# Optimization experiments

Measured on AMD Instinct MI355X. Metric: run time of the kernel, lower is better.

Reference implementation:

```python
import jax, jax.numpy as jnp
import numpy as np

THRESH = 0.5
MARGIN = 0.1
SCALE_POS = 2.0
SCALE_NEG = 40.0
EPS = 1e-5


def setup_inputs() -> dict:
    key = jax.random.key(0)
    k1, k2 = jax.random.split(key)
    B, D, NUM_CLASSES = 4096, 512, 512
    feats = jax.random.normal(k1, (B, D), dtype=jnp.float32)
    feats = feats / jnp.linalg.norm(feats, axis=1, keepdims=True)  # unit-norm embeddings
    labels = jax.random.randint(k2, (B,), 0, NUM_CLASSES, dtype=jnp.int64)
    return {"feats": feats, "labels": labels, "label_num": 26}


def reference(feats, labels, label_num):
    B = feats.shape[0]
    sim = feats @ feats.T  # [B, B]
    same = labels[:, None] == labels[None, :]
    pos_m = same & (sim < 1.0 - EPS)      # pos_pair_ mask per row
    neg_m = ~same                         # neg_pair_ mask per row
    has_pos = pos_m.any(axis=1)
    has_neg = neg_m.any(axis=1)
    min_pos = jnp.min(jnp.where(pos_m, sim, jnp.inf), axis=1)
    max_neg = jnp.max(jnp.where(neg_m, sim, -jnp.inf), axis=1)
    pos_thr = jnp.where(has_pos, min_pos, jnp.float32(0.2))  # fallback when no pos pairs
    neg_thr = jnp.where(has_neg, max_neg, jnp.float32(0.8))  # fallback when no neg pairs
    # mined pairs (same semantics as the per-row boolean filtering)
    neg_pair = neg_m & (sim + MARGIN > pos_thr[:, None])
    pos_pair = pos_m & (sim - MARGIN < neg_thr[:, None])
    valid = pos_pair.any(axis=1) & neg_pair.any(axis=1) & (jnp.arange(B) < B - label_num)
    # masked log-sum-exp style reductions (exp of -inf on masked entries -> 0)
    pos_sum = jnp.sum(jnp.exp(jnp.where(pos_pair, -SCALE_POS * (sim - THRESH), -jnp.inf)), axis=1)
    neg_sum = jnp.sum(jnp.exp(jnp.where(neg_pair, SCALE_NEG * (sim - THRESH), -jnp.inf)), axis=1)
    per_row = (1.0 / SCALE_POS) * jnp.log1p(pos_sum) + (1.0 / SCALE_NEG) * jnp.log1p(neg_sum)
    return jnp.sum(jnp.where(valid, per_row, 0.0)) / B
```

## Files before the change

### kernel.cpp

```cpp
#include <hip/hip_runtime.h>
#include <stdint.h>

#define BN 4096
#define DK 512
#define THRESH 0.5f
#define MARGIN 0.1f

typedef __attribute__((ext_vector_type(8))) __bf16 bf16x8;
typedef __attribute__((ext_vector_type(4))) float f32x4;
typedef __attribute__((ext_vector_type(8))) unsigned short ushort8;

__device__ __forceinline__ unsigned short f2bf(float f) {
    unsigned u = __float_as_uint(f);
    u += 0x7FFFu + ((u >> 16) & 1u);
    return (unsigned short)(u >> 16);
}
__device__ __forceinline__ float bf2f(unsigned short b) {
    return __uint_as_float((unsigned)b << 16);
}

__device__ __forceinline__ void async_cp16(void* lds, const void* g) {
    __builtin_amdgcn_global_load_lds(
        (const __attribute__((address_space(1))) void*)g,
        (__attribute__((address_space(3))) void*)lds,
        16, 0, 0);
}

__global__ void cvt_kernel(const float4* __restrict__ in, ushort4* __restrict__ out,
                           float* __restrict__ loss_out) {
    int i = blockIdx.x * blockDim.x + threadIdx.x;
    float4 v = in[i];
    ushort4 o;
    o.x = f2bf(v.x); o.y = f2bf(v.y); o.z = f2bf(v.z); o.w = f2bf(v.w);
    out[i] = o;
    if (blockIdx.x == 0 && threadIdx.x == 0) loss_out[0] = 0.f;
}

__global__ __launch_bounds__(256, 4) void ms_gemm(
    const unsigned short* __restrict__ Fb,
    unsigned short* __restrict__ simb)
{
    __shared__ __align__(16) unsigned short SMEM[2 * 128 * 64];
    unsigned short* As = SMEM;
    unsigned short* Bs = SMEM + 128 * 64;

    const int t    = threadIdx.x;
    const int lane = t & 63;
    const int w    = t >> 6;
    const int wr   = w >> 1, wc = w & 1;
    const int quad = lane >> 4;
    const int cIdx = lane & 15;

    int l = blockIdx.x, by = 0;
    while (l >= 32 - by) { l -= (32 - by); ++by; }
    const int bx = by + l;
    const int rowBase = by * 128;
    const int colBase = bx * 128;

    f32x4 acc[4][4];
#pragma unroll
    for (int i = 0; i < 4; ++i)
#pragma unroll
        for (int j = 0; j < 4; ++j) acc[i][j] = (f32x4){0.f, 0.f, 0.f, 0.f};

    const int lrow   = t >> 3;
    const int swz    = (t & 7) ^ (lrow & 7);
    const int ldsOff = t * 8;

    for (int k0 = 0; k0 < DK; k0 += 64) {
#pragma unroll
        for (int it = 0; it < 4; ++it) {
            const unsigned short* gA =
                Fb + (size_t)(rowBase + it * 32 + lrow) * DK + k0 + swz * 8;
            async_cp16(&As[it * 2048 + ldsOff], gA);
        }
#pragma unroll
        for (int it = 0; it < 4; ++it) {
            const unsigned short* gB =
                Fb + (size_t)(colBase + it * 32 + lrow) * DK + k0 + swz * 8;
            async_cp16(&Bs[it * 2048 + ldsOff], gB);
        }
        __syncthreads();

#pragma unroll
        for (int kk = 0; kk < 2; ++kk) {
            bf16x8 af[4], bg[4];
#pragma unroll
            for (int im = 0; im < 4; ++im) {
                int r = wr * 64 + im * 16 + cIdx;
                int p = (kk * 4 + quad) ^ (r & 7);
                af[im] = *reinterpret_cast<const bf16x8*>(&As[r * 64 + p * 8]);
            }
#pragma unroll
            for (int jn = 0; jn < 4; ++jn) {
                int c = wc * 64 + jn * 16 + cIdx;
                int p = (kk * 4 + quad) ^ (c & 7);
                bg[jn] = *reinterpret_cast<const bf16x8*>(&Bs[c * 64 + p * 8]);
            }
#pragma unroll
            for (int im = 0; im < 4; ++im)
#pragma unroll
                for (int jn = 0; jn < 4; ++jn)
                    acc[im][jn] = __builtin_amdgcn_mfma_f32_16x16x32_bf16(
                        af[im], bg[jn], acc[im][jn], 0, 0, 0);
        }
        __syncthreads();
    }

#pragma unroll
    for (int im = 0; im < 4; ++im)
#pragma unroll
        for (int rg = 0; rg < 4; ++rg) {
            const int grow = rowBase + wr * 64 + im * 16 + quad * 4 + rg;
            unsigned short* dst = simb + (size_t)grow * BN + colBase + wc * 64 + cIdx;
#pragma unroll
            for (int jn = 0; jn < 4; ++jn)
                dst[jn * 16] = f2bf(acc[im][jn][rg]);
        }

    if (by == bx) return;

#pragma unroll
    for (int im = 0; im < 4; ++im)
#pragma unroll
        for (int jn = 0; jn < 4; ++jn) {
            ushort4 v;
            v.x = f2bf(acc[im][jn][0]);
            v.y = f2bf(acc[im][jn][1]);
            v.z = f2bf(acc[im][jn][2]);
            v.w = f2bf(acc[im][jn][3]);
            const int c  = wc * 64 + jn * 16 + cIdx;
            const int r  = wr * 64 + im * 16 + quad * 4;
            const int r8 = r >> 3;
            const int ri = r & 7;
            *reinterpret_cast<ushort4*>(
                &SMEM[c * 128 + ((r8 ^ (c & 15)) << 3) + ri]) = v;
        }
    __syncthreads();

    const int lch = t & 7;
    const int trw = t >> 3;
#pragma unroll
    for (int it = 0; it < 4; ++it) {
        const int tr = it * 32 + trw;
        const int q1 = lch ^ (tr & 15);
        const int q2 = (lch + 8) ^ (tr & 15);
        ushort8 a = *reinterpret_cast<const ushort8*>(&SMEM[tr * 128 + q1 * 8]);
        ushort8 b = *reinterpret_cast<const ushort8*>(&SMEM[tr * 128 + q2 * 8]);
        unsigned short* dst = simb + (size_t)(colBase + tr) * BN + rowBase;
        *reinterpret_cast<ushort8*>(&dst[lch * 8])       = a;
        *reinterpret_cast<ushort8*>(&dst[(lch + 8) * 8]) = b;
    }
}

__global__ __launch_bounds__(256) void ms_rows(
    const unsigned short* __restrict__ simb,
    const int* __restrict__ labels,
    const int* __restrict__ label_num,
    float* __restrict__ out)
{
    __shared__ int   labS[BN];
    __shared__ float bsum[4];

    const int t    = threadIdx.x;
    const int lane = t & 63;
    const int w    = t >> 6;

    for (int i = t; i < BN; i += 256) labS[i] = labels[i];
    __syncthreads();

    const int lim = BN - label_num[0];
    const int row = blockIdx.x * 4 + w;
    const int lr  = labS[row];
    const ushort8* rp = (const ushort8*)(simb + (size_t)row * BN);

    ushort8 d[8];
    uint64_t mpos = 0, msame = 0;
    float mn = INFINITY, mx = -INFINITY;
#pragma unroll
    for (int j = 0; j < 8; ++j) {
        d[j] = rp[j * 64 + lane];
#pragma unroll
        for (int e = 0; e < 8; ++e) {
            const int col = (j * 64 + lane) * 8 + e;
            const float s = bf2f(d[j][e]);
            const bool same = (labS[col] == lr);
            const bool pos  = same && (col != row);
            if (pos)   mn = fminf(mn, s);
            if (!same) mx = fmaxf(mx, s);
            msame |= (uint64_t)same << (j * 8 + e);
            mpos  |= (uint64_t)pos  << (j * 8 + e);
        }
    }
#pragma unroll
    for (int off = 1; off < 64; off <<= 1) {
        mn = fminf(mn, __shfl_xor(mn, off, 64));
        mx = fmaxf(mx, __shfl_xor(mx, off, 64));
    }
    const float tP = (mn < 1e30f)  ? mn : 0.2f;
    const float tN = (mx > -1e30f) ? mx : 0.8f;

    float ps = 0.f, ns = 0.f;
#pragma unroll
    for (int j = 0; j < 8; ++j)
#pragma unroll
        for (int e = 0; e < 8; ++e) {
            const int k = j * 8 + e;
            const float s = bf2f(d[j][e]);
            if (((mpos >> k) & 1) && (s - MARGIN < tN))
                ps += __expf(-2.0f * (s - THRESH));
            if (!((msame >> k) & 1) && (s + MARGIN > tP))
                ns += __expf(40.0f * (s - THRESH));
        }
#pragma unroll
    for (int off = 1; off < 64; off <<= 1) {
        ps += __shfl_xor(ps, off, 64);
        ns += __shfl_xor(ns, off, 64);
    }
    float wsum = 0.f;
    if (lane == 0 && ps > 0.f && ns > 0.f && row < lim)
        wsum = 0.5f * log1pf(ps) + 0.025f * log1pf(ns);

    if (lane == 0) bsum[w] = wsum;
    __syncthreads();
    if (t == 0)
        atomicAdd(out, (bsum[0] + bsum[1] + bsum[2] + bsum[3]) * (1.0f / (float)BN));
}

extern "C" void kernel_launch(void* const* d_in, const int* in_sizes, int n_in,
                              void* d_out, int out_size, void* d_ws, size_t ws_size,
                              hipStream_t stream)
{
    const float* feats     = (const float*)d_in[0];
    const int*   labels    = (const int*)d_in[1];
    const int*   label_num = (const int*)d_in[2];
    float*       out       = (float*)d_out;

    char* ws = (char*)d_ws;
    unsigned short* Fb   = (unsigned short*)ws;
    unsigned short* simb = (unsigned short*)(ws + 4u * 1024u * 1024u);

    cvt_kernel<<<2048, 256, 0, stream>>>((const float4*)feats, (ushort4*)Fb, out);

    ms_gemm<<<528, 256, 0, stream>>>(Fb, simb);

    ms_rows<<<1024, 256, 0, stream>>>(simb, labels, label_num, out);
}
```

Measured before the change: 112.2 us.

## Skip redundant B-tile loads on diagonal blocks and prune negligible negative exps

```diff
diff --git a/kernel.cpp b/kernel.cpp
--- a/kernel.cpp
+++ b/kernel.cpp
@@ -56,6 +56,8 @@
     const int bx = by + l;
     const int rowBase = by * 128;
     const int colBase = bx * 128;
+    const bool diag = (by == bx);
+    const unsigned short* Bsel = diag ? As : Bs;
 
     f32x4 acc[4][4];
 #pragma unroll
@@ -74,11 +76,13 @@
                 Fb + (size_t)(rowBase + it * 32 + lrow) * DK + k0 + swz * 8;
             async_cp16(&As[it * 2048 + ldsOff], gA);
         }
-#pragma unroll
-        for (int it = 0; it < 4; ++it) {
-            const unsigned short* gB =
-                Fb + (size_t)(colBase + it * 32 + lrow) * DK + k0 + swz * 8;
-            async_cp16(&Bs[it * 2048 + ldsOff], gB);
+        if (!diag) {
+#pragma unroll
+            for (int it = 0; it < 4; ++it) {
+                const unsigned short* gB =
+                    Fb + (size_t)(colBase + it * 32 + lrow) * DK + k0 + swz * 8;
+                async_cp16(&Bs[it * 2048 + ldsOff], gB);
+            }
         }
         __syncthreads();
 
@@ -95,7 +99,7 @@
             for (int jn = 0; jn < 4; ++jn) {
                 int c = wc * 64 + jn * 16 + cIdx;
                 int p = (kk * 4 + quad) ^ (c & 7);
-                bg[jn] = *reinterpret_cast<const bf16x8*>(&Bs[c * 64 + p * 8]);
+                bg[jn] = *reinterpret_cast<const bf16x8*>(&Bsel[c * 64 + p * 8]);
             }
 #pragma unroll
             for (int im = 0; im < 4; ++im)
@@ -118,7 +122,7 @@
                 dst[jn * 16] = f2bf(acc[im][jn][rg]);
         }
 
-    if (by == bx) return;
+    if (diag) return;
 
 #pragma unroll
     for (int im = 0; im < 4; ++im)
@@ -159,19 +163,19 @@
     const int* __restrict__ label_num,
     float* __restrict__ out)
 {
-    __shared__ int   labS[BN];
+    __shared__ int   labT[8][512];
     __shared__ float bsum[4];
 
     const int t    = threadIdx.x;
     const int lane = t & 63;
     const int w    = t >> 6;
 
-    for (int i = t; i < BN; i += 256) labS[i] = labels[i];
+    for (int i = t; i < BN; i += 256) labT[i & 7][i >> 3] = labels[i];
     __syncthreads();
 
     const int lim = BN - label_num[0];
     const int row = blockIdx.x * 4 + w;
-    const int lr  = labS[row];
+    const int lr  = labT[row & 7][row >> 3];
     const ushort8* rp = (const ushort8*)(simb + (size_t)row * BN);
 
     ushort8 d[8];
@@ -180,11 +184,12 @@
 #pragma unroll
     for (int j = 0; j < 8; ++j) {
         d[j] = rp[j * 64 + lane];
+        const int c8 = j * 64 + lane;
 #pragma unroll
         for (int e = 0; e < 8; ++e) {
-            const int col = (j * 64 + lane) * 8 + e;
+            const int col = c8 * 8 + e;
             const float s = bf2f(d[j][e]);
-            const bool same = (labS[col] == lr);
+            const bool same = (labT[e][c8] == lr);
             const bool pos  = same && (col != row);
             if (pos)   mn = fminf(mn, s);
             if (!same) mx = fmaxf(mx, s);
@@ -201,24 +206,30 @@
     const float tN = (mx > -1e30f) ? mx : 0.8f;
 
     float ps = 0.f, ns = 0.f;
+    bool anyN = false;
 #pragma unroll
     for (int j = 0; j < 8; ++j)
 #pragma unroll
         for (int e = 0; e < 8; ++e) {
             const int k = j * 8 + e;
             const float s = bf2f(d[j][e]);
-            if (((mpos >> k) & 1) && (s - MARGIN < tN))
-                ps += __expf(-2.0f * (s - THRESH));
-            if (!((msame >> k) & 1) && (s + MARGIN > tP))
-                ns += __expf(40.0f * (s - THRESH));
+            const bool doP = ((mpos >> k) & 1) && (s - MARGIN < tN);
+            if (__any(doP))
+                ps += doP ? __expf(-2.0f * (s - THRESH)) : 0.f;
+            const bool doN = !((msame >> k) & 1) && (s + MARGIN > tP);
+            anyN |= doN;
+            const bool doNe = doN && (s > 0.125f);
+            if (__any(doNe))
+                ns += doNe ? __expf(40.0f * (s - THRESH)) : 0.f;
         }
 #pragma unroll
     for (int off = 1; off < 64; off <<= 1) {
         ps += __shfl_xor(ps, off, 64);
         ns += __shfl_xor(ns, off, 64);
     }
+    const bool anyNw = __any(anyN);
     float wsum = 0.f;
-    if (lane == 0 && ps > 0.f && ns > 0.f && row < lim)
+    if (lane == 0 && ps > 0.f && anyNw && row < lim)
         wsum = 0.5f * log1pf(ps) + 0.025f * log1pf(ns);
 
     if (lane == 0) bsum[w] = wsum;
```

Result: no change. 111.9 us (-0.3%).
